# Optimization experiments

Hardware: AMD Instinct MI355X
Metric: run time of the kernel (lower is better)

Reference implementation:

```python
import jax, jax.numpy as jnp
import numpy as np

EPS = 1e-7  # K.epsilon()
ROUTINGS = 3

def squash(v, axis=-1):
    s2 = jnp.sum(jnp.square(v), axis=axis, keepdims=True)
    scale = s2 / (1.0 + s2) / jnp.sqrt(s2 + EPS)
    return scale * v

def setup_inputs() -> dict:
    key = jax.random.key(0)
    k1, k2 = jax.random.split(key)
    B, N, I = 128, 512, 256   # batch, input_num_capsule, input_dim_capsule
    M, D = 32, 16             # num_capsule, dim_capsule
    x = jax.random.normal(k1, (B, N, I), dtype=jnp.float32)
    W = jax.random.normal(k2, (M, N, D, I), dtype=jnp.float32) * 0.05
    return {"x": x, "W": W}

def reference(x, W):
    # x: [B,N,I], W: [M,N,D,I]
    # inputs_hat[b,m,n,d] = sum_i x[b,n,i] * W[m,n,d,i]
    inputs_hat = jnp.einsum('bni,mndi->bmnd', x, W)
    B, M, N, _ = inputs_hat.shape
    b = jnp.zeros((B, M, N), dtype=inputs_hat.dtype)
    outputs = None
    for i in range(ROUTINGS):
        c = jax.nn.softmax(b, axis=1)  # softmax over num_capsule dim (dim=1)
        s = jnp.einsum('bmn,bmnd->bmd', c, inputs_hat)
        outputs = squash(s)
        if i < ROUTINGS - 1:
            b = b + jnp.einsum('bmd,bmnd->bmn', outputs, inputs_hat)
    return outputs
```

## Files before the change

kernel.cpp:

```cpp
#include <hip/hip_runtime.h>
#include <hip/hip_bf16.h>
#include <stdint.h>

#define B_ 128
#define N_ 512
#define I_ 256
#define M_ 32
#define D_ 16

typedef __attribute__((ext_vector_type(4))) float f32x4;
typedef __attribute__((ext_vector_type(4))) float float4v;
typedef __attribute__((ext_vector_type(8))) short short8;
typedef __attribute__((ext_vector_type(4))) unsigned short ushort4v;

__device__ __forceinline__ float bf2f(unsigned short u) {
    union { unsigned int i; float f; } v; v.i = ((unsigned int)u) << 16; return v.f;
}
__device__ __forceinline__ unsigned short f2bf(float f) {
    union { float f; unsigned int i; } v; v.f = f;
    unsigned int r = v.i + 0x7FFFu + ((v.i >> 16) & 1u);
    return (unsigned short)(r >> 16);
}

#define LDK 72

__global__ __launch_bounds__(256) void hat_gemm(const float* __restrict__ x,
                                                const float* __restrict__ W,
                                                unsigned short* __restrict__ hat) {
    __shared__ unsigned short As[128][LDK];
    __shared__ unsigned short Bs[128][LDK];

    const int n    = blockIdx.y;
    const int mc   = blockIdx.x;
    const int tid  = threadIdx.x;
    const int lane = tid & 63;
    const int w    = tid >> 6;

    const int sgrp  = tid >> 4;
    const int klane = (tid & 15) * 4;

    const float* xbase = x + ((size_t)sgrp * N_ + n) * I_ + klane;
    const float* wbase = W + (((size_t)(mc * 8) * N_ + n) * D_ + sgrp) * I_ + klane;

    const size_t xstep = (size_t)16 * N_ * I_;
    const size_t wstep = (size_t)N_ * D_ * I_;

    float4v pa[8], pb[8];

    f32x4 acc[2][8];
    #pragma unroll
    for (int a = 0; a < 2; ++a)
        #pragma unroll
        for (int c = 0; c < 8; ++c) { f32x4 z = {0.f, 0.f, 0.f, 0.f}; acc[a][c] = z; }

    #pragma unroll
    for (int r = 0; r < 8; ++r) {
        pa[r] = *(const float4v*)(xbase + (size_t)r * xstep);
        pb[r] = *(const float4v*)(wbase + (size_t)r * wstep);
    }

    for (int kt = 0; kt < 4; ++kt) {
        #pragma unroll
        for (int r = 0; r < 8; ++r) {
            ushort4v ha, hb;
            ha[0] = f2bf(pa[r][0]); ha[1] = f2bf(pa[r][1]);
            ha[2] = f2bf(pa[r][2]); ha[3] = f2bf(pa[r][3]);
            hb[0] = f2bf(pb[r][0]); hb[1] = f2bf(pb[r][1]);
            hb[2] = f2bf(pb[r][2]); hb[3] = f2bf(pb[r][3]);
            *(ushort4v*)&As[r * 16 + sgrp][klane] = ha;
            *(ushort4v*)&Bs[r * 16 + sgrp][klane] = hb;
        }
        __syncthreads();

        if (kt < 3) {
            const int k0 = (kt + 1) * 64;
            #pragma unroll
            for (int r = 0; r < 8; ++r) {
                pa[r] = *(const float4v*)(xbase + (size_t)r * xstep + k0);
                pb[r] = *(const float4v*)(wbase + (size_t)r * wstep + k0);
            }
        }

        #pragma unroll
        for (int ks = 0; ks < 2; ++ks) {
            const int kb = ks * 32 + ((lane >> 4) << 3);
            short8 a0 = *(const short8*)&As[w * 32 +      (lane & 15)][kb];
            short8 a1 = *(const short8*)&As[w * 32 + 16 + (lane & 15)][kb];
            #pragma unroll
            for (int ct = 0; ct < 8; ++ct) {
                short8 bb = *(const short8*)&Bs[ct * 16 + (lane & 15)][kb];
                acc[0][ct] = __builtin_amdgcn_mfma_f32_16x16x32_bf16(a0, bb, acc[0][ct], 0, 0, 0);
                acc[1][ct] = __builtin_amdgcn_mfma_f32_16x16x32_bf16(a1, bb, acc[1][ct], 0, 0, 0);
            }
        }
        __syncthreads();
    }

    const int d  = lane & 15;
    const int rq = lane >> 4;
    #pragma unroll
    for (int rt = 0; rt < 2; ++rt) {
        #pragma unroll
        for (int ct = 0; ct < 8; ++ct) {
            const int m = mc * 8 + ct;
            #pragma unroll
            for (int r = 0; r < 4; ++r) {
                const int brow = w * 32 + rt * 16 + rq * 4 + r;
                const size_t idx = (((size_t)brow * M_ + m) * N_ + n) * D_ + d;
                hat[idx] = f2bf(acc[rt][ct][r]);
            }
        }
    }
}

__global__ __launch_bounds__(512) void routing(const unsigned short* __restrict__ hat,
                                               float* __restrict__ out) {
    __shared__ float blog[M_][N_];
    __shared__ float cmax[N_];
    __shared__ float rcsum[N_];

    const int b    = blockIdx.x;
    const int tid  = threadIdx.x;
    const int lane = tid & 63;
    const int w    = tid >> 6;

    #pragma unroll
    for (int m = 0; m < M_; ++m) blog[m][tid] = 0.f;
    __syncthreads();

    float ov[4][16];

    for (int it = 0; it < 3; ++it) {
        {
            float mx = -3.4e38f;
            #pragma unroll
            for (int m = 0; m < M_; ++m) mx = fmaxf(mx, blog[m][tid]);
            float s = 0.f;
            #pragma unroll
            for (int m = 0; m < M_; ++m) s += __expf(blog[m][tid] - mx);
            cmax[tid]  = mx;
            rcsum[tid] = 1.f / s;
        }
        __syncthreads();

        float sacc[4][16];
        #pragma unroll
        for (int q = 0; q < 4; ++q)
            #pragma unroll
            for (int dd = 0; dd < 16; ++dd) sacc[q][dd] = 0.f;

        for (int r = 0; r < 8; ++r) {
            const int nn = r * 64 + lane;
            #pragma unroll
            for (int q = 0; q < 4; ++q) {
                const int m = w * 4 + q;
                const float cm = __expf(blog[m][nn] - cmax[nn]) * rcsum[nn];
                const size_t base = (((size_t)b * M_ + m) * N_ + nn) * D_;
                short8 h0 = *(const short8*)(hat + base);
                short8 h1 = *(const short8*)(hat + base + 8);
                #pragma unroll
                for (int dd = 0; dd < 8; ++dd) {
                    sacc[q][dd]     += cm * bf2f((unsigned short)h0[dd]);
                    sacc[q][8 + dd] += cm * bf2f((unsigned short)h1[dd]);
                }
            }
        }
        #pragma unroll
        for (int off = 32; off >= 1; off >>= 1) {
            #pragma unroll
            for (int q = 0; q < 4; ++q)
                #pragma unroll
                for (int dd = 0; dd < 16; ++dd)
                    sacc[q][dd] += __shfl_xor(sacc[q][dd], off, 64);
        }
        #pragma unroll
        for (int q = 0; q < 4; ++q) {
            float s2 = 0.f;
            #pragma unroll
            for (int dd = 0; dd < 16; ++dd) s2 += sacc[q][dd] * sacc[q][dd];
            const float scale = s2 / (1.f + s2) / sqrtf(s2 + 1e-7f);
            #pragma unroll
            for (int dd = 0; dd < 16; ++dd) ov[q][dd] = scale * sacc[q][dd];
        }

        if (it < 2) {
            for (int r = 0; r < 8; ++r) {
                const int nn = r * 64 + lane;
                #pragma unroll
                for (int q = 0; q < 4; ++q) {
                    const int m = w * 4 + q;
                    const size_t base = (((size_t)b * M_ + m) * N_ + nn) * D_;
                    short8 h0 = *(const short8*)(hat + base);
                    short8 h1 = *(const short8*)(hat + base + 8);
                    float dot = 0.f;
                    #pragma unroll
                    for (int dd = 0; dd < 8; ++dd) {
                        dot += ov[q][dd]     * bf2f((unsigned short)h0[dd]);
                        dot += ov[q][8 + dd] * bf2f((unsigned short)h1[dd]);
                    }
                    blog[m][nn] += dot;
                }
            }
        }
        __syncthreads();
    }

    if (lane == 0) {
        #pragma unroll
        for (int q = 0; q < 4; ++q) {
            const int m = w * 4 + q;
            #pragma unroll
            for (int c4 = 0; c4 < 4; ++c4) {
                float4v v;
                v[0] = ov[q][c4 * 4 + 0];
                v[1] = ov[q][c4 * 4 + 1];
                v[2] = ov[q][c4 * 4 + 2];
                v[3] = ov[q][c4 * 4 + 3];
                *(float4v*)&out[((size_t)b * M_ + m) * D_ + c4 * 4] = v;
            }
        }
    }
}

extern "C" void kernel_launch(void* const* d_in, const int* in_sizes, int n_in,
                              void* d_out, int out_size, void* d_ws, size_t ws_size,
                              hipStream_t stream) {
    const float* x = (const float*)d_in[0];
    const float* W = (const float*)d_in[1];
    unsigned short* hat = (unsigned short*)d_ws;
    float* out = (float*)d_out;

    dim3 g1(4, N_);
    hat_gemm<<<g1, dim3(256), 0, stream>>>(x, W, hat);
    routing<<<dim3(B_), dim3(512), 0, stream>>>(hat, out);
}
```

Before: 190.4 us.

## Halve GEMM column tile and remap blocks so each XCD shares x rows

The hat_gemm column tile shrinks from 8 to 4 output capsules per block, doubling the grid to 4096 blocks and cutting registers and LDS per block. A linear block index is remapped so blocks on the same XCD (index mod 8) cover a contiguous range of n, improving L2 reuse of x across the m-chunks. The cost is that each x tile is now loaded and converted by twice as many blocks.

```diff
diff --git a/kernel.cpp b/kernel.cpp
--- a/kernel.cpp
+++ b/kernel.cpp
@@ -1,5 +1,4 @@
 #include <hip/hip_runtime.h>
-#include <hip/hip_bf16.h>
 #include <stdint.h>
 
 #define B_ 128
@@ -28,67 +27,75 @@
                                                 const float* __restrict__ W,
                                                 unsigned short* __restrict__ hat) {
     __shared__ unsigned short As[128][LDK];
-    __shared__ unsigned short Bs[128][LDK];
-
-    const int n    = blockIdx.y;
-    const int mc   = blockIdx.x;
+    __shared__ unsigned short Bs[64][LDK];
+
+    const int L   = blockIdx.x;
+    const int xcd = L & 7;
+    const int i   = L >> 3;
+    const int n   = xcd * 64 + (i >> 3);
+    const int mc  = i & 7;
+
     const int tid  = threadIdx.x;
     const int lane = tid & 63;
     const int w    = tid >> 6;
+    const int l15  = lane & 15;
 
     const int sgrp  = tid >> 4;
     const int klane = (tid & 15) * 4;
 
-    const float* xbase = x + ((size_t)sgrp * N_ + n) * I_ + klane;
-    const float* wbase = W + (((size_t)(mc * 8) * N_ + n) * D_ + sgrp) * I_ + klane;
-
+    const float* xrow = x + ((size_t)sgrp * N_ + n) * I_ + klane;
+    const float* wrow = W + (((size_t)(mc * 4) * N_ + n) * D_ + sgrp) * I_ + klane;
     const size_t xstep = (size_t)16 * N_ * I_;
     const size_t wstep = (size_t)N_ * D_ * I_;
 
-    float4v pa[8], pb[8];
-
-    f32x4 acc[2][8];
+    float4v pa[8], pb[4];
+
+    f32x4 acc[2][4];
     #pragma unroll
     for (int a = 0; a < 2; ++a)
         #pragma unroll
-        for (int c = 0; c < 8; ++c) { f32x4 z = {0.f, 0.f, 0.f, 0.f}; acc[a][c] = z; }
-
-    #pragma unroll
-    for (int r = 0; r < 8; ++r) {
-        pa[r] = *(const float4v*)(xbase + (size_t)r * xstep);
-        pb[r] = *(const float4v*)(wbase + (size_t)r * wstep);
-    }
+        for (int c = 0; c < 4; ++c) { f32x4 z = {0.f, 0.f, 0.f, 0.f}; acc[a][c] = z; }
+
+    #pragma unroll
+    for (int r = 0; r < 8; ++r) pa[r] = *(const float4v*)(xrow + (size_t)r * xstep);
+    #pragma unroll
+    for (int r = 0; r < 4; ++r) pb[r] = *(const float4v*)(wrow + (size_t)r * wstep);
 
     for (int kt = 0; kt < 4; ++kt) {
         #pragma unroll
         for (int r = 0; r < 8; ++r) {
-            ushort4v ha, hb;
-            ha[0] = f2bf(pa[r][0]); ha[1] = f2bf(pa[r][1]);
-            ha[2] = f2bf(pa[r][2]); ha[3] = f2bf(pa[r][3]);
-            hb[0] = f2bf(pb[r][0]); hb[1] = f2bf(pb[r][1]);
-            hb[2] = f2bf(pb[r][2]); hb[3] = f2bf(pb[r][3]);
-            *(ushort4v*)&As[r * 16 + sgrp][klane] = ha;
-            *(ushort4v*)&Bs[r * 16 + sgrp][klane] = hb;
+            ushort4v h;
+            h[0] = f2bf(pa[r][0]); h[1] = f2bf(pa[r][1]);
+            h[2] = f2bf(pa[r][2]); h[3] = f2bf(pa[r][3]);
+            *(ushort4v*)&As[r * 16 + sgrp][klane] = h;
+        }
+        #pragma unroll
+        for (int r = 0; r < 4; ++r) {
+            ushort4v h;
+            h[0] = f2bf(pb[r][0]); h[1] = f2bf(pb[r][1]);
+            h[2] = f2bf(pb[r][2]); h[3] = f2bf(pb[r][3]);
+            *(ushort4v*)&Bs[r * 16 + sgrp][klane] = h;
         }
         __syncthreads();
 
         if (kt < 3) {
             const int k0 = (kt + 1) * 64;
             #pragma unroll
-            for (int r = 0; r < 8; ++r) {
-                pa[r] = *(const float4v*)(xbase + (size_t)r * xstep + k0);
-                pb[r] = *(const float4v*)(wbase + (size_t)r * wstep + k0);
-            }
+            for (int r = 0; r < 8; ++r)
+                pa[r] = *(const float4v*)(xrow + (size_t)r * xstep + k0);
+            #pragma unroll
+            for (int r = 0; r < 4; ++r)
+                pb[r] = *(const float4v*)(wrow + (size_t)r * wstep + k0);
         }
 
         #pragma unroll
         for (int ks = 0; ks < 2; ++ks) {
             const int kb = ks * 32 + ((lane >> 4) << 3);
-            short8 a0 = *(const short8*)&As[w * 32 +      (lane & 15)][kb];
-            short8 a1 = *(const short8*)&As[w * 32 + 16 + (lane & 15)][kb];
-            #pragma unroll
-            for (int ct = 0; ct < 8; ++ct) {
-                short8 bb = *(const short8*)&Bs[ct * 16 + (lane & 15)][kb];
+            short8 a0 = *(const short8*)&As[w * 32 +      l15][kb];
+            short8 a1 = *(const short8*)&As[w * 32 + 16 + l15][kb];
+            #pragma unroll
+            for (int ct = 0; ct < 4; ++ct) {
+                short8 bb = *(const short8*)&Bs[ct * 16 + l15][kb];
                 acc[0][ct] = __builtin_amdgcn_mfma_f32_16x16x32_bf16(a0, bb, acc[0][ct], 0, 0, 0);
                 acc[1][ct] = __builtin_amdgcn_mfma_f32_16x16x32_bf16(a1, bb, acc[1][ct], 0, 0, 0);
             }
@@ -96,13 +103,13 @@
         __syncthreads();
     }
 
-    const int d  = lane & 15;
+    const int d  = l15;
     const int rq = lane >> 4;
     #pragma unroll
     for (int rt = 0; rt < 2; ++rt) {
         #pragma unroll
-        for (int ct = 0; ct < 8; ++ct) {
-            const int m = mc * 8 + ct;
+        for (int ct = 0; ct < 4; ++ct) {
+            const int m = mc * 4 + ct;
             #pragma unroll
             for (int r = 0; r < 4; ++r) {
                 const int brow = w * 32 + rt * 16 + rq * 4 + r;
@@ -230,7 +237,6 @@
     unsigned short* hat = (unsigned short*)d_ws;
     float* out = (float*)d_out;
 
-    dim3 g1(4, N_);
-    hat_gemm<<<g1, dim3(256), 0, stream>>>(x, W, hat);
+    hat_gemm<<<dim3(4096), dim3(256), 0, stream>>>(x, W, hat);
     routing<<<dim3(B_), dim3(512), 0, stream>>>(hat, out);
 }
```

Measured after the change: 187.1 us. Within noise of the previous version (-1.7%).
